# Kernel tuning notes

Hardware: AMD Instinct MI355X
Metric: run time of the kernel (lower is better)

Reference implementation:

```python
import jax, jax.numpy as jnp
import numpy as np
from jax.scipy.special import logsumexp

EPS = 0.1
MAX_ITER = 10
THRESH = 0.1


def setup_inputs() -> dict:
    key = jax.random.key(0)
    k1, k2 = jax.random.split(key)
    N, P, D = 16, 1024, 64
    y = jax.random.normal(k1, (N, P, D), dtype=jnp.float32)
    x = jax.random.normal(k2, (N, P, D), dtype=jnp.float32)
    return {"y": y, "x": x}


def reference(y, x):
    # Cost matrix |x_i - y_j|^2 summed over feature dim: (N, P1, P2)
    C = jnp.sum(jnp.abs(x[:, :, None, :] - y[:, None, :, :]) ** 2, axis=-1)
    N, P1, P2 = C.shape
    mu = jnp.full((N, P1), 1.0 / P1, dtype=C.dtype)
    nu = jnp.full((N, P2), 1.0 / P2, dtype=C.dtype)

    def M(u, v):
        # (-C + u_i + v_j) / eps
        return (-C + u[:, :, None] + v[:, None, :]) / EPS

    def body(carry, _):
        u, v, done = carry
        u_new = EPS * (jnp.log(mu + 1e-8) - logsumexp(M(u, v), axis=-1)) + u
        v_new = EPS * (jnp.log(nu + 1e-8) - logsumexp(M(u_new, v), axis=-2)) + v
        err = jnp.abs(u_new - u).sum(-1).mean()
        # emulate torch's early break: freeze updates once converged
        u2 = jnp.where(done, u, u_new)
        v2 = jnp.where(done, v, v_new)
        done2 = done | (err < THRESH)
        return (u2, v2, done2), None

    u0 = jnp.zeros_like(mu)
    v0 = jnp.zeros_like(nu)
    (u, v, _), _ = jax.lax.scan(body, (u0, v0, jnp.array(False)), None, length=MAX_ITER)
    pi = jnp.exp(M(u, v))  # transport plan (N, P1, P2)
    return pi
```

## Files before the change

### kernel.cpp

```cpp
#include <hip/hip_runtime.h>
#include <math.h>

#define NB 16
#define PP 1024
#define DD 64
#define MAX_ITER 10
#define RCH 16
#define NCH (PP / RCH)
#define NBLK (NB * NCH)
#define CH (NB * PP)

constexpr float EPSV    = 0.1f;
constexpr float SCALE_G = 20.0f;
constexpr float LOG2E   = 1.44269504088896340736f;
constexpr float LOG_MU  = -6.93146156597137f;
constexpr float THRESHV = 0.1f;

typedef short bf16x8 __attribute__((ext_vector_type(8)));
typedef float f32x16 __attribute__((ext_vector_type(16)));

__device__ __forceinline__ unsigned short f2bf(float f) {
  unsigned int u = __float_as_uint(f);
  return (unsigned short)((u + 0x7FFFu + ((u >> 16) & 1u)) >> 16);
}
__device__ __forceinline__ float bf2f(unsigned short h) {
  return __uint_as_float(((unsigned int)h) << 16);
}

__device__ __forceinline__ const bf16x8* frag(const unsigned short* pk, int g, int q, int l) {
  return (const bf16x8*)(pk + (((size_t)g * 4 + q) * 64 + l) * 8);
}

__global__ __launch_bounds__(256) void prep_kernel(
    const float* __restrict__ x, const float* __restrict__ y,
    unsigned short* __restrict__ xhp, unsigned short* __restrict__ xlp,
    unsigned short* __restrict__ yhp, unsigned short* __restrict__ ylp,
    float* __restrict__ nxs, float* __restrict__ nys)
{
  const int sel = blockIdx.x >> 9;
  const int row = (blockIdx.x & 511) * 32 + (threadIdx.x >> 3);
  const int q   = threadIdx.x & 7;

  const float* src = sel ? y : x;
  unsigned short* H = sel ? yhp : xhp;
  unsigned short* L = sel ? ylp : xlp;
  float* N          = sel ? nys : nxs;

  const float* p = src + (size_t)row * DD + q * 8;
  float4 v0 = *(const float4*)(p);
  float4 v1 = *(const float4*)(p + 4);

  float f[8] = {v0.x, v0.y, v0.z, v0.w, v1.x, v1.y, v1.z, v1.w};
  float nrm = 0.f;
  unsigned short hb[8], lb[8];
  #pragma unroll
  for (int k = 0; k < 8; ++k) {
    nrm = fmaf(f[k], f[k], nrm);
    unsigned short h = f2bf(f[k]);
    float res = f[k] - bf2f(h);
    hb[k] = h; lb[k] = f2bf(res);
  }
  nrm += __shfl_xor(nrm, 1);
  nrm += __shfl_xor(nrm, 2);
  nrm += __shfl_xor(nrm, 4);
  if (q == 0) N[row] = 10.0f * nrm;

  uint4 ho, lo;
  ho.x = hb[0] | ((unsigned)hb[1] << 16); ho.y = hb[2] | ((unsigned)hb[3] << 16);
  ho.z = hb[4] | ((unsigned)hb[5] << 16); ho.w = hb[6] | ((unsigned)hb[7] << 16);
  lo.x = lb[0] | ((unsigned)lb[1] << 16); lo.y = lb[2] | ((unsigned)lb[3] << 16);
  lo.z = lb[4] | ((unsigned)lb[5] << 16); lo.w = lb[6] | ((unsigned)lb[7] << 16);

  const int grp  = row >> 5;
  const int lane = (row & 31) + 32 * (q & 1);
  const size_t dst = (((size_t)grp * 4 + (q >> 1)) * 64 + lane) * 8;
  *(uint4*)(H + dst) = ho;
  *(uint4*)(L + dst) = lo;
}

__global__ __launch_bounds__(256) void compute_c_mfma(
    const unsigned short* __restrict__ xhp, const unsigned short* __restrict__ xlp,
    const float* __restrict__ nxs,
    const unsigned short* __restrict__ yhp, const unsigned short* __restrict__ ylp,
    const float* __restrict__ nys,
    float* __restrict__ Cs)
{
  const int n   = blockIdx.x & 15;
  const int ib  = (blockIdx.x >> 4) & 15;
  const int jb  = blockIdx.x >> 8;
  const int tid = threadIdx.x;
  const int l   = tid & 63;
  const int w   = tid >> 6;
  const int ih  = w & 1, jh = w >> 1;

  __shared__ float nxv[64];
  if (tid < 64) nxv[tid] = nxs[n * PP + ib * 64 + tid];
  __syncthreads();

  const int jg  = n * PP + jb * 64 + 32 * jh + (l & 31);
  const float nyv = nys[jg];

  const int gX = n * 32 + ib * 2 + ih;
  const int gY = n * 32 + jb * 2 + jh;

  f32x16 acc;
  #pragma unroll
  for (int z = 0; z < 16; ++z) acc[z] = 0.f;
  #pragma unroll
  for (int q = 0; q < 4; ++q) {
    bf16x8 Xh = *frag(xhp, gX, q, l);
    bf16x8 Xl = *frag(xlp, gX, q, l);
    bf16x8 Yh = *frag(yhp, gY, q, l);
    bf16x8 Yl = *frag(ylp, gY, q, l);
    acc = __builtin_amdgcn_mfma_f32_32x32x16_bf16(Xh, Yh, acc, 0, 0, 0);
    acc = __builtin_amdgcn_mfma_f32_32x32x16_bf16(Xh, Yl, acc, 0, 0, 0);
    acc = __builtin_amdgcn_mfma_f32_32x32x16_bf16(Xl, Yh, acc, 0, 0, 0);
  }

  const int irb  = 32 * ih + 4 * (l >> 5);
  const int jcol = jb * 64 + 32 * jh + (l & 31);
  #pragma unroll
  for (int r = 0; r < 16; ++r) {
    const int irel = irb + (r & 3) + 8 * (r >> 2);
    const size_t off = ((size_t)(n * PP + ib * 64 + irel)) * PP + jcol;
    Cs[off] = nxv[irel] + nyv - SCALE_G * acc[r];
  }
}

__global__ __launch_bounds__(256, 4) void iter_fused(
    const float* __restrict__ Cs, float* __restrict__ aG, const float* __restrict__ bG,
    float* __restrict__ pm, float* __restrict__ ps, float* __restrict__ errBlk,
    const int* __restrict__ doneFlags, int it)
{
  if (it > 0 && doneFlags[it - 1]) return;

  const int n   = blockIdx.x & 15;
  const int rc  = blockIdx.x >> 4;
  const int tid = threadIdx.x;
  const int l   = tid & 63;
  const int wv  = tid >> 6;

  __shared__ float bb[PP];
  __shared__ float aArr[RCH];
  __shared__ float dsum[RCH];

  if (it == 0) {
    *(float4*)&bb[tid * 4] = make_float4(0.f, 0.f, 0.f, 0.f);
  } else {
    *(float4*)&bb[tid * 4] = *(const float4*)(bG + n * PP + tid * 4);
  }
  __syncthreads();

  const int rbase = rc * RCH + 4 * wv;
  const float* cbase = Cs + ((size_t)(n * PP + rbase)) * PP;

  float4 bbv[4];
  #pragma unroll
  for (int s = 0; s < 4; ++s) bbv[s] = *(const float4*)&bb[s * 256 + l * 4];

  float4 tv[16];
  #pragma unroll
  for (int t = 0; t < 16; ++t) {
    const int r = t >> 2, s = t & 3;
    float4 c4 = *(const float4*)(cbase + (size_t)r * PP + s * 256 + l * 4);
    tv[t] = make_float4(bbv[s].x - c4.x, bbv[s].y - c4.y,
                        bbv[s].z - c4.z, bbv[s].w - c4.w);
  }

  float m0 = -INFINITY, m1 = -INFINITY, m2 = -INFINITY, m3 = -INFINITY;
  #pragma unroll
  for (int s = 0; s < 4; ++s) {
    m0 = fmaxf(m0, fmaxf(fmaxf(tv[s].x, tv[s].y), fmaxf(tv[s].z, tv[s].w)));
    m1 = fmaxf(m1, fmaxf(fmaxf(tv[4+s].x, tv[4+s].y), fmaxf(tv[4+s].z, tv[4+s].w)));
    m2 = fmaxf(m2, fmaxf(fmaxf(tv[8+s].x, tv[8+s].y), fmaxf(tv[8+s].z, tv[8+s].w)));
    m3 = fmaxf(m3, fmaxf(fmaxf(tv[12+s].x, tv[12+s].y), fmaxf(tv[12+s].z, tv[12+s].w)));
  }
  #pragma unroll
  for (int mask = 32; mask; mask >>= 1) {
    m0 = fmaxf(m0, __shfl_xor(m0, mask));
    m1 = fmaxf(m1, __shfl_xor(m1, mask));
    m2 = fmaxf(m2, __shfl_xor(m2, mask));
    m3 = fmaxf(m3, __shfl_xor(m3, mask));
  }

  float s0 = 0.f, s1 = 0.f, s2 = 0.f, s3 = 0.f;
  #pragma unroll
  for (int s = 0; s < 4; ++s) {
    s0 += exp2f((tv[s].x - m0) * LOG2E) + exp2f((tv[s].y - m0) * LOG2E)
        + exp2f((tv[s].z - m0) * LOG2E) + exp2f((tv[s].w - m0) * LOG2E);
    s1 += exp2f((tv[4+s].x - m1) * LOG2E) + exp2f((tv[4+s].y - m1) * LOG2E)
        + exp2f((tv[4+s].z - m1) * LOG2E) + exp2f((tv[4+s].w - m1) * LOG2E);
    s2 += exp2f((tv[8+s].x - m2) * LOG2E) + exp2f((tv[8+s].y - m2) * LOG2E)
        + exp2f((tv[8+s].z - m2) * LOG2E) + exp2f((tv[8+s].w - m2) * LOG2E);
    s3 += exp2f((tv[12+s].x - m3) * LOG2E) + exp2f((tv[12+s].y - m3) * LOG2E)
        + exp2f((tv[12+s].z - m3) * LOG2E) + exp2f((tv[12+s].w - m3) * LOG2E);
  }
  #pragma unroll
  for (int mask = 32; mask; mask >>= 1) {
    s0 += __shfl_xor(s0, mask);
    s1 += __shfl_xor(s1, mask);
    s2 += __shfl_xor(s2, mask);
    s3 += __shfl_xor(s3, mask);
  }

  if (l == 0) {
    float mg[4] = {m0, m1, m2, m3};
    float sg[4] = {s0, s1, s2, s3};
    #pragma unroll
    for (int g = 0; g < 4; ++g) {
      const int row = n * PP + rbase + g;
      float aOld = (it == 0) ? 0.f : aG[row];
      float an = LOG_MU - (mg[g] + logf(sg[g]));
      aG[row] = an;
      aArr[4 * wv + g] = an;
      dsum[4 * wv + g] = fabsf(an - aOld);
    }
  }
  __syncthreads();
  if (tid == 0) {
    float e = 0.f;
    #pragma unroll
    for (int r = 0; r < RCH; ++r) e += dsum[r];
    errBlk[blockIdx.x] = e;
  }

  const int c0 = tid * 4;
  const float* cb = Cs + ((size_t)(n * PP + rc * RCH)) * PP + c0;

  float cm0 = -INFINITY, cm1 = -INFINITY, cm2 = -INFINITY, cm3 = -INFINITY;
  #pragma unroll
  for (int r = 0; r < RCH; ++r) {
    float ar = aArr[r];
    float4 c4 = *(const float4*)(cb + (size_t)r * PP);
    cm0 = fmaxf(cm0, ar - c4.x);
    cm1 = fmaxf(cm1, ar - c4.y);
    cm2 = fmaxf(cm2, ar - c4.z);
    cm3 = fmaxf(cm3, ar - c4.w);
  }
  float cs0 = 0.f, cs1 = 0.f, cs2 = 0.f, cs3 = 0.f;
  #pragma unroll
  for (int r = 0; r < RCH; ++r) {
    float ar = aArr[r];
    float4 c4 = *(const float4*)(cb + (size_t)r * PP);
    cs0 += exp2f((ar - c4.x - cm0) * LOG2E);
    cs1 += exp2f((ar - c4.y - cm1) * LOG2E);
    cs2 += exp2f((ar - c4.z - cm2) * LOG2E);
    cs3 += exp2f((ar - c4.w - cm3) * LOG2E);
  }
  size_t off = ((size_t)(n * NCH + rc)) * PP + c0;
  *(float4*)(pm + off) = make_float4(cm0, cm1, cm2, cm3);
  *(float4*)(ps + off) = make_float4(cs0, cs1, cs2, cs3);
}

__global__ __launch_bounds__(256) void v_combine(
    const float* __restrict__ pm, const float* __restrict__ ps,
    float* __restrict__ bG, const float* __restrict__ errBlk,
    int* __restrict__ doneFlags, int it)
{
  if (it > 0 && doneFlags[it - 1]) {
    if (blockIdx.x == 0 && threadIdx.x == 0) doneFlags[it] = 1;
    return;
  }
  const int col = blockIdx.x * 256 + threadIdx.x;
  const int n = col >> 10, j = col & (PP - 1);
  const float* pmn = pm + (size_t)n * NCH * PP + j;
  const float* psn = ps + (size_t)n * NCH * PP + j;

  float m = -INFINITY, s = 0.f;
  #pragma unroll 8
  for (int c = 0; c < NCH; ++c) {
    float mc = pmn[(size_t)c * PP];
    float sc = psn[(size_t)c * PP];
    float mn = fmaxf(m, mc);
    s = fmaf(s, exp2f((m - mn) * LOG2E), sc * exp2f((mc - mn) * LOG2E));
    m = mn;
  }
  bG[col] = LOG_MU - (m + logf(s));

  if (blockIdx.x == 0) {
    __shared__ float red[4];
    float loc = 0.f;
    for (int t = threadIdx.x; t < NBLK; t += 256) loc += errBlk[t];
    #pragma unroll
    for (int off = 32; off > 0; off >>= 1) loc += __shfl_xor(loc, off);
    if ((threadIdx.x & 63) == 0) red[threadIdx.x >> 6] = loc;
    __syncthreads();
    if (threadIdx.x == 0) {
      float tot = red[0] + red[1] + red[2] + red[3];
      float err = tot * (EPSV / (float)NB);
      doneFlags[it] = (err < THRESHV) ? 1 : 0;
    }
  }
}

__global__ __launch_bounds__(256) void pi_mfma(
    const unsigned short* __restrict__ xhp, const unsigned short* __restrict__ xlp,
    const unsigned short* __restrict__ yhp, const unsigned short* __restrict__ ylp,
    const float* __restrict__ aG, const float* __restrict__ bG,
    const float* __restrict__ nxs, const float* __restrict__ nys,
    float* __restrict__ pi)
{
  const int n   = blockIdx.x & 15;
  const int ib  = (blockIdx.x >> 4) & 15;
  const int jb  = blockIdx.x >> 8;
  const int tid = threadIdx.x;
  const int l   = tid & 63;
  const int w   = tid >> 6;
  const int ih  = w & 1, jh = w >> 1;

  __shared__ float atv[64];
  if (tid < 64) {
    int gi = n * PP + ib * 64 + tid;
    atv[tid] = aG[gi] - nxs[gi];
  }
  __syncthreads();

  const int jg  = n * PP + jb * 64 + 32 * jh + (l & 31);
  const float btv = bG[jg] - nys[jg];

  const int gX = n * 32 + ib * 2 + ih;
  const int gY = n * 32 + jb * 2 + jh;

  f32x16 acc;
  #pragma unroll
  for (int z = 0; z < 16; ++z) acc[z] = 0.f;
  #pragma unroll
  for (int q = 0; q < 4; ++q) {
    bf16x8 Xh = *frag(xhp, gX, q, l);
    bf16x8 Xl = *frag(xlp, gX, q, l);
    bf16x8 Yh = *frag(yhp, gY, q, l);
    bf16x8 Yl = *frag(ylp, gY, q, l);
    acc = __builtin_amdgcn_mfma_f32_32x32x16_bf16(Xh, Yh, acc, 0, 0, 0);
    acc = __builtin_amdgcn_mfma_f32_32x32x16_bf16(Xh, Yl, acc, 0, 0, 0);
    acc = __builtin_amdgcn_mfma_f32_32x32x16_bf16(Xl, Yh, acc, 0, 0, 0);
  }

  const int irb  = 32 * ih + 4 * (l >> 5);
  const int jcol = jb * 64 + 32 * jh + (l & 31);
  #pragma unroll
  for (int r = 0; r < 16; ++r) {
    const int irel = irb + (r & 3) + 8 * (r >> 2);
    const size_t off = ((size_t)(n * PP + ib * 64 + irel)) * PP + jcol;
    pi[off] = exp2f((atv[irel] + btv + SCALE_G * acc[r]) * LOG2E);
  }
}

extern "C" void kernel_launch(void* const* d_in, const int* in_sizes, int n_in,
                              void* d_out, int out_size, void* d_ws, size_t ws_size,
                              hipStream_t stream)
{
  const float* y = (const float*)d_in[0];
  const float* x = (const float*)d_in[1];

  float* Cs = (float*)d_out;

  const size_t NE = (size_t)NB * PP * DD;
  unsigned short* xhp = (unsigned short*)d_ws;
  unsigned short* xlp = xhp + NE;
  unsigned short* yhp = xlp + NE;
  unsigned short* ylp = yhp + NE;
  float* pm = (float*)d_ws;
  float* ps = pm + (size_t)NB * NCH * PP;

  float* tail   = (float*)((char*)d_ws + 4 * NE * sizeof(unsigned short));
  float* nxs    = tail;
  float* nys    = nxs + CH;
  float* aG     = nys + CH;
  float* bG     = aG + CH;
  float* errBlk = bG + CH;
  int*   doneFl = (int*)(errBlk + NBLK);

  prep_kernel<<<1024, 256, 0, stream>>>(x, y, xhp, xlp, yhp, ylp, nxs, nys);
  compute_c_mfma<<<4096, 256, 0, stream>>>(xhp, xlp, nxs, yhp, ylp, nys, Cs);
  for (int it = 0; it < MAX_ITER; ++it) {
    iter_fused<<<NBLK, 256, 0, stream>>>(Cs, aG, bG, pm, ps, errBlk, doneFl, it);
    v_combine<<<NB * PP / 256, 256, 0, stream>>>(pm, ps, bG, errBlk, doneFl, it);
  }
  prep_kernel<<<1024, 256, 0, stream>>>(x, y, xhp, xlp, yhp, ylp, nxs, nys);
  pi_mfma<<<4096, 256, 0, stream>>>(xhp, xlp, yhp, ylp, aG, bG, nxs, nys, Cs);
}
```

Measured before the change: 365.7 us.

## Reuse register-held cost rows for column logsumexp partials via LDS reduction

```diff
diff --git a/kernel.cpp b/kernel.cpp
--- a/kernel.cpp
+++ b/kernel.cpp
@@ -141,6 +141,8 @@
   const int wv  = tid >> 6;
 
   __shared__ float bb[PP];
+  __shared__ float pmL[4][PP];
+  __shared__ float psL[4][PP];
   __shared__ float aArr[RCH];
   __shared__ float dsum[RCH];
 
@@ -224,32 +226,67 @@
     errBlk[blockIdx.x] = e;
   }
 
-  const int c0 = tid * 4;
-  const float* cb = Cs + ((size_t)(n * PP + rc * RCH)) * PP + c0;
-
-  float cm0 = -INFINITY, cm1 = -INFINITY, cm2 = -INFINITY, cm3 = -INFINITY;
-  #pragma unroll
-  for (int r = 0; r < RCH; ++r) {
-    float ar = aArr[r];
-    float4 c4 = *(const float4*)(cb + (size_t)r * PP);
-    cm0 = fmaxf(cm0, ar - c4.x);
-    cm1 = fmaxf(cm1, ar - c4.y);
-    cm2 = fmaxf(cm2, ar - c4.z);
-    cm3 = fmaxf(cm3, ar - c4.w);
-  }
-  float cs0 = 0.f, cs1 = 0.f, cs2 = 0.f, cs3 = 0.f;
-  #pragma unroll
-  for (int r = 0; r < RCH; ++r) {
-    float ar = aArr[r];
-    float4 c4 = *(const float4*)(cb + (size_t)r * PP);
-    cs0 += exp2f((ar - c4.x - cm0) * LOG2E);
-    cs1 += exp2f((ar - c4.y - cm1) * LOG2E);
-    cs2 += exp2f((ar - c4.z - cm2) * LOG2E);
-    cs3 += exp2f((ar - c4.w - cm3) * LOG2E);
-  }
-  size_t off = ((size_t)(n * NCH + rc)) * PP + c0;
-  *(float4*)(pm + off) = make_float4(cm0, cm1, cm2, cm3);
-  *(float4*)(ps + off) = make_float4(cs0, cs1, cs2, cs3);
+  float a4[4];
+  #pragma unroll
+  for (int g = 0; g < 4; ++g) a4[g] = aArr[4 * wv + g];
+
+  #pragma unroll
+  for (int s = 0; s < 4; ++s) {
+    float4 q0 = tv[s], q1 = tv[4 + s], q2 = tv[8 + s], q3 = tv[12 + s];
+    float4 b4 = bbv[s];
+    float4 c0 = make_float4(a4[0] - b4.x + q0.x, a4[0] - b4.y + q0.y,
+                            a4[0] - b4.z + q0.z, a4[0] - b4.w + q0.w);
+    float4 c1 = make_float4(a4[1] - b4.x + q1.x, a4[1] - b4.y + q1.y,
+                            a4[1] - b4.z + q1.z, a4[1] - b4.w + q1.w);
+    float4 c2 = make_float4(a4[2] - b4.x + q2.x, a4[2] - b4.y + q2.y,
+                            a4[2] - b4.z + q2.z, a4[2] - b4.w + q2.w);
+    float4 c3 = make_float4(a4[3] - b4.x + q3.x, a4[3] - b4.y + q3.y,
+                            a4[3] - b4.z + q3.z, a4[3] - b4.w + q3.w);
+    float4 mm = make_float4(fmaxf(fmaxf(c0.x, c1.x), fmaxf(c2.x, c3.x)),
+                            fmaxf(fmaxf(c0.y, c1.y), fmaxf(c2.y, c3.y)),
+                            fmaxf(fmaxf(c0.z, c1.z), fmaxf(c2.z, c3.z)),
+                            fmaxf(fmaxf(c0.w, c1.w), fmaxf(c2.w, c3.w)));
+    float4 ss;
+    ss.x = exp2f((c0.x - mm.x) * LOG2E) + exp2f((c1.x - mm.x) * LOG2E)
+         + exp2f((c2.x - mm.x) * LOG2E) + exp2f((c3.x - mm.x) * LOG2E);
+    ss.y = exp2f((c0.y - mm.y) * LOG2E) + exp2f((c1.y - mm.y) * LOG2E)
+         + exp2f((c2.y - mm.y) * LOG2E) + exp2f((c3.y - mm.y) * LOG2E);
+    ss.z = exp2f((c0.z - mm.z) * LOG2E) + exp2f((c1.z - mm.z) * LOG2E)
+         + exp2f((c2.z - mm.z) * LOG2E) + exp2f((c3.z - mm.z) * LOG2E);
+    ss.w = exp2f((c0.w - mm.w) * LOG2E) + exp2f((c1.w - mm.w) * LOG2E)
+         + exp2f((c2.w - mm.w) * LOG2E) + exp2f((c3.w - mm.w) * LOG2E);
+    *(float4*)&pmL[wv][s * 256 + l * 4] = mm;
+    *(float4*)&psL[wv][s * 256 + l * 4] = ss;
+  }
+  __syncthreads();
+
+  {
+    const int c0i = tid * 4;
+    float4 M0 = *(const float4*)&pmL[0][c0i];
+    float4 M1 = *(const float4*)&pmL[1][c0i];
+    float4 M2 = *(const float4*)&pmL[2][c0i];
+    float4 M3 = *(const float4*)&pmL[3][c0i];
+    float4 S0 = *(const float4*)&psL[0][c0i];
+    float4 S1 = *(const float4*)&psL[1][c0i];
+    float4 S2 = *(const float4*)&psL[2][c0i];
+    float4 S3 = *(const float4*)&psL[3][c0i];
+    float4 MM, SS;
+    MM.x = fmaxf(fmaxf(M0.x, M1.x), fmaxf(M2.x, M3.x));
+    MM.y = fmaxf(fmaxf(M0.y, M1.y), fmaxf(M2.y, M3.y));
+    MM.z = fmaxf(fmaxf(M0.z, M1.z), fmaxf(M2.z, M3.z));
+    MM.w = fmaxf(fmaxf(M0.w, M1.w), fmaxf(M2.w, M3.w));
+    SS.x = S0.x * exp2f((M0.x - MM.x) * LOG2E) + S1.x * exp2f((M1.x - MM.x) * LOG2E)
+         + S2.x * exp2f((M2.x - MM.x) * LOG2E) + S3.x * exp2f((M3.x - MM.x) * LOG2E);
+    SS.y = S0.y * exp2f((M0.y - MM.y) * LOG2E) + S1.y * exp2f((M1.y - MM.y) * LOG2E)
+         + S2.y * exp2f((M2.y - MM.y) * LOG2E) + S3.y * exp2f((M3.y - MM.y) * LOG2E);
+    SS.z = S0.z * exp2f((M0.z - MM.z) * LOG2E) + S1.z * exp2f((M1.z - MM.z) * LOG2E)
+         + S2.z * exp2f((M2.z - MM.z) * LOG2E) + S3.z * exp2f((M3.z - MM.z) * LOG2E);
+    SS.w = S0.w * exp2f((M0.w - MM.w) * LOG2E) + S1.w * exp2f((M1.w - MM.w) * LOG2E)
+         + S2.w * exp2f((M2.w - MM.w) * LOG2E) + S3.w * exp2f((M3.w - MM.w) * LOG2E);
+    size_t off = ((size_t)(n * NCH + rc)) * PP + c0i;
+    *(float4*)(pm + off) = MM;
+    *(float4*)(ps + off) = SS;
+  }
 }
 
 __global__ __launch_bounds__(256) void v_combine(
```

New measurement: 366.4 us. Within noise of the previous version (+0.2%).

## Compute column logsumexp partials from registers, avoiding a second cost-matrix read

Applied to the files above, without the earlier changes.

```diff
diff --git a/kernel.cpp b/kernel.cpp
--- a/kernel.cpp
+++ b/kernel.cpp
@@ -5,9 +5,9 @@
 #define PP 1024
 #define DD 64
 #define MAX_ITER 10
-#define RCH 16
-#define NCH (PP / RCH)
-#define NBLK (NB * NCH)
+#define RB 64
+#define NCHK (PP / RB)
+#define NBLK2 (NB * NCHK)
 #define CH (NB * PP)
 
 constexpr float EPSV    = 0.1f;
@@ -127,7 +127,7 @@
   }
 }
 
-__global__ __launch_bounds__(256, 4) void iter_fused(
+__global__ __launch_bounds__(512, 4) void iter_fused(
     const float* __restrict__ Cs, float* __restrict__ aG, const float* __restrict__ bG,
     float* __restrict__ pm, float* __restrict__ ps, float* __restrict__ errBlk,
     const int* __restrict__ doneFlags, int it)
@@ -141,115 +141,150 @@
   const int wv  = tid >> 6;
 
   __shared__ float bb[PP];
-  __shared__ float aArr[RCH];
-  __shared__ float dsum[RCH];
-
-  if (it == 0) {
-    *(float4*)&bb[tid * 4] = make_float4(0.f, 0.f, 0.f, 0.f);
-  } else {
-    *(float4*)&bb[tid * 4] = *(const float4*)(bG + n * PP + tid * 4);
+  __shared__ float pmL[8][PP + 8];
+  __shared__ float psL[8][PP + 8];
+  __shared__ float aArr[RB];
+  __shared__ float dsum[RB];
+
+  if (tid < 256) {
+    if (it == 0) {
+      *(float4*)&bb[tid * 4] = make_float4(0.f, 0.f, 0.f, 0.f);
+    } else {
+      *(float4*)&bb[tid * 4] = *(const float4*)(bG + n * PP + tid * 4);
+    }
   }
   __syncthreads();
 
-  const int rbase = rc * RCH + 4 * wv;
+  const int rbase = rc * RB + 8 * wv;
   const float* cbase = Cs + ((size_t)(n * PP + rbase)) * PP;
 
   float4 bbv[4];
   #pragma unroll
   for (int s = 0; s < 4; ++s) bbv[s] = *(const float4*)&bb[s * 256 + l * 4];
 
-  float4 tv[16];
-  #pragma unroll
-  for (int t = 0; t < 16; ++t) {
-    const int r = t >> 2, s = t & 3;
-    float4 c4 = *(const float4*)(cbase + (size_t)r * PP + s * 256 + l * 4);
-    tv[t] = make_float4(bbv[s].x - c4.x, bbv[s].y - c4.y,
-                        bbv[s].z - c4.z, bbv[s].w - c4.w);
-  }
-
-  float m0 = -INFINITY, m1 = -INFINITY, m2 = -INFINITY, m3 = -INFINITY;
+  float cm[16], cs[16];
+  #pragma unroll
+  for (int t = 0; t < 16; ++t) { cm[t] = -INFINITY; cs[t] = 0.f; }
+
+  #pragma unroll
+  for (int g = 0; g < 2; ++g) {
+    float4 tv[16];
+    #pragma unroll
+    for (int t = 0; t < 16; ++t) {
+      const int r = t >> 2, s = t & 3;
+      float4 c4 = *(const float4*)(cbase + (size_t)(4 * g + r) * PP + s * 256 + l * 4);
+      tv[t] = make_float4(bbv[s].x - c4.x, bbv[s].y - c4.y,
+                          bbv[s].z - c4.z, bbv[s].w - c4.w);
+    }
+
+    float m0 = -INFINITY, m1 = -INFINITY, m2 = -INFINITY, m3 = -INFINITY;
+    #pragma unroll
+    for (int s = 0; s < 4; ++s) {
+      m0 = fmaxf(m0, fmaxf(fmaxf(tv[s].x, tv[s].y), fmaxf(tv[s].z, tv[s].w)));
+      m1 = fmaxf(m1, fmaxf(fmaxf(tv[4+s].x, tv[4+s].y), fmaxf(tv[4+s].z, tv[4+s].w)));
+      m2 = fmaxf(m2, fmaxf(fmaxf(tv[8+s].x, tv[8+s].y), fmaxf(tv[8+s].z, tv[8+s].w)));
+      m3 = fmaxf(m3, fmaxf(fmaxf(tv[12+s].x, tv[12+s].y), fmaxf(tv[12+s].z, tv[12+s].w)));
+    }
+    #pragma unroll
+    for (int mask = 32; mask; mask >>= 1) {
+      m0 = fmaxf(m0, __shfl_xor(m0, mask));
+      m1 = fmaxf(m1, __shfl_xor(m1, mask));
+      m2 = fmaxf(m2, __shfl_xor(m2, mask));
+      m3 = fmaxf(m3, __shfl_xor(m3, mask));
+    }
+    float s0 = 0.f, s1 = 0.f, s2 = 0.f, s3 = 0.f;
+    #pragma unroll
+    for (int s = 0; s < 4; ++s) {
+      s0 += exp2f((tv[s].x - m0) * LOG2E) + exp2f((tv[s].y - m0) * LOG2E)
+          + exp2f((tv[s].z - m0) * LOG2E) + exp2f((tv[s].w - m0) * LOG2E);
+      s1 += exp2f((tv[4+s].x - m1) * LOG2E) + exp2f((tv[4+s].y - m1) * LOG2E)
+          + exp2f((tv[4+s].z - m1) * LOG2E) + exp2f((tv[4+s].w - m1) * LOG2E);
+      s2 += exp2f((tv[8+s].x - m2) * LOG2E) + exp2f((tv[8+s].y - m2) * LOG2E)
+          + exp2f((tv[8+s].z - m2) * LOG2E) + exp2f((tv[8+s].w - m2) * LOG2E);
+      s3 += exp2f((tv[12+s].x - m3) * LOG2E) + exp2f((tv[12+s].y - m3) * LOG2E)
+          + exp2f((tv[12+s].z - m3) * LOG2E) + exp2f((tv[12+s].w - m3) * LOG2E);
+    }
+    #pragma unroll
+    for (int mask = 32; mask; mask >>= 1) {
+      s0 += __shfl_xor(s0, mask);
+      s1 += __shfl_xor(s1, mask);
+      s2 += __shfl_xor(s2, mask);
+      s3 += __shfl_xor(s3, mask);
+    }
+
+    float an[4];
+    an[0] = LOG_MU - (m0 + logf(s0));
+    an[1] = LOG_MU - (m1 + logf(s1));
+    an[2] = LOG_MU - (m2 + logf(s2));
+    an[3] = LOG_MU - (m3 + logf(s3));
+
+    if (l == 0) {
+      #pragma unroll
+      for (int r = 0; r < 4; ++r) {
+        const int lrow = 8 * wv + 4 * g + r;
+        const int grow = n * PP + rc * RB + lrow;
+        float aOld = (it == 0) ? 0.f : aG[grow];
+        aG[grow] = an[r];
+        aArr[lrow] = an[r];
+        dsum[lrow] = fabsf(an[r] - aOld);
+      }
+    }
+
+    #pragma unroll
+    for (int s = 0; s < 4; ++s) {
+      float4 q0 = tv[s], q1 = tv[4 + s], q2 = tv[8 + s], q3 = tv[12 + s];
+      float4 b4 = bbv[s];
+      float bc[4] = {b4.x, b4.y, b4.z, b4.w};
+      float t0[4] = {q0.x, q0.y, q0.z, q0.w};
+      float t1[4] = {q1.x, q1.y, q1.z, q1.w};
+      float t2[4] = {q2.x, q2.y, q2.z, q2.w};
+      float t3[4] = {q3.x, q3.y, q3.z, q3.w};
+      #pragma unroll
+      for (int k = 0; k < 4; ++k) {
+        float c0 = an[0] - bc[k] + t0[k];
+        float c1 = an[1] - bc[k] + t1[k];
+        float c2 = an[2] - bc[k] + t2[k];
+        float c3 = an[3] - bc[k] + t3[k];
+        float mn = fmaxf(fmaxf(c0, c1), fmaxf(c2, c3));
+        float sn = exp2f((c0 - mn) * LOG2E) + exp2f((c1 - mn) * LOG2E)
+                 + exp2f((c2 - mn) * LOG2E) + exp2f((c3 - mn) * LOG2E);
+        const int idx = s * 4 + k;
+        float M = fmaxf(cm[idx], mn);
+        cs[idx] = cs[idx] * exp2f((cm[idx] - M) * LOG2E) + sn * exp2f((mn - M) * LOG2E);
+        cm[idx] = M;
+      }
+    }
+  }
+
   #pragma unroll
   for (int s = 0; s < 4; ++s) {
-    m0 = fmaxf(m0, fmaxf(fmaxf(tv[s].x, tv[s].y), fmaxf(tv[s].z, tv[s].w)));
-    m1 = fmaxf(m1, fmaxf(fmaxf(tv[4+s].x, tv[4+s].y), fmaxf(tv[4+s].z, tv[4+s].w)));
-    m2 = fmaxf(m2, fmaxf(fmaxf(tv[8+s].x, tv[8+s].y), fmaxf(tv[8+s].z, tv[8+s].w)));
-    m3 = fmaxf(m3, fmaxf(fmaxf(tv[12+s].x, tv[12+s].y), fmaxf(tv[12+s].z, tv[12+s].w)));
-  }
-  #pragma unroll
-  for (int mask = 32; mask; mask >>= 1) {
-    m0 = fmaxf(m0, __shfl_xor(m0, mask));
-    m1 = fmaxf(m1, __shfl_xor(m1, mask));
-    m2 = fmaxf(m2, __shfl_xor(m2, mask));
-    m3 = fmaxf(m3, __shfl_xor(m3, mask));
-  }
-
-  float s0 = 0.f, s1 = 0.f, s2 = 0.f, s3 = 0.f;
-  #pragma unroll
-  for (int s = 0; s < 4; ++s) {
-    s0 += exp2f((tv[s].x - m0) * LOG2E) + exp2f((tv[s].y - m0) * LOG2E)
-        + exp2f((tv[s].z - m0) * LOG2E) + exp2f((tv[s].w - m0) * LOG2E);
-    s1 += exp2f((tv[4+s].x - m1) * LOG2E) + exp2f((tv[4+s].y - m1) * LOG2E)
-        + exp2f((tv[4+s].z - m1) * LOG2E) + exp2f((tv[4+s].w - m1) * LOG2E);
-    s2 += exp2f((tv[8+s].x - m2) * LOG2E) + exp2f((tv[8+s].y - m2) * LOG2E)
-        + exp2f((tv[8+s].z - m2) * LOG2E) + exp2f((tv[8+s].w - m2) * LOG2E);
-    s3 += exp2f((tv[12+s].x - m3) * LOG2E) + exp2f((tv[12+s].y - m3) * LOG2E)
-        + exp2f((tv[12+s].z - m3) * LOG2E) + exp2f((tv[12+s].w - m3) * LOG2E);
-  }
-  #pragma unroll
-  for (int mask = 32; mask; mask >>= 1) {
-    s0 += __shfl_xor(s0, mask);
-    s1 += __shfl_xor(s1, mask);
-    s2 += __shfl_xor(s2, mask);
-    s3 += __shfl_xor(s3, mask);
-  }
-
-  if (l == 0) {
-    float mg[4] = {m0, m1, m2, m3};
-    float sg[4] = {s0, s1, s2, s3};
-    #pragma unroll
-    for (int g = 0; g < 4; ++g) {
-      const int row = n * PP + rbase + g;
-      float aOld = (it == 0) ? 0.f : aG[row];
-      float an = LOG_MU - (mg[g] + logf(sg[g]));
-      aG[row] = an;
-      aArr[4 * wv + g] = an;
-      dsum[4 * wv + g] = fabsf(an - aOld);
-    }
+    *(float4*)&pmL[wv][s * 256 + l * 4] = make_float4(cm[s*4+0], cm[s*4+1], cm[s*4+2], cm[s*4+3]);
+    *(float4*)&psL[wv][s * 256 + l * 4] = make_float4(cs[s*4+0], cs[s*4+1], cs[s*4+2], cs[s*4+3]);
   }
   __syncthreads();
+
   if (tid == 0) {
     float e = 0.f;
     #pragma unroll
-    for (int r = 0; r < RCH; ++r) e += dsum[r];
+    for (int r = 0; r < RB; ++r) e += dsum[r];
     errBlk[blockIdx.x] = e;
   }
 
-  const int c0 = tid * 4;
-  const float* cb = Cs + ((size_t)(n * PP + rc * RCH)) * PP + c0;
-
-  float cm0 = -INFINITY, cm1 = -INFINITY, cm2 = -INFINITY, cm3 = -INFINITY;
-  #pragma unroll
-  for (int r = 0; r < RCH; ++r) {
-    float ar = aArr[r];
-    float4 c4 = *(const float4*)(cb + (size_t)r * PP);
-    cm0 = fmaxf(cm0, ar - c4.x);
-    cm1 = fmaxf(cm1, ar - c4.y);
-    cm2 = fmaxf(cm2, ar - c4.z);
-    cm3 = fmaxf(cm3, ar - c4.w);
-  }
-  float cs0 = 0.f, cs1 = 0.f, cs2 = 0.f, cs3 = 0.f;
-  #pragma unroll
-  for (int r = 0; r < RCH; ++r) {
-    float ar = aArr[r];
-    float4 c4 = *(const float4*)(cb + (size_t)r * PP);
-    cs0 += exp2f((ar - c4.x - cm0) * LOG2E);
-    cs1 += exp2f((ar - c4.y - cm1) * LOG2E);
-    cs2 += exp2f((ar - c4.z - cm2) * LOG2E);
-    cs3 += exp2f((ar - c4.w - cm3) * LOG2E);
-  }
-  size_t off = ((size_t)(n * NCH + rc)) * PP + c0;
-  *(float4*)(pm + off) = make_float4(cm0, cm1, cm2, cm3);
-  *(float4*)(ps + off) = make_float4(cs0, cs1, cs2, cs3);
+  {
+    #pragma unroll
+    for (int u = 0; u < 2; ++u) {
+      const int j = tid * 2 + u;
+      float M = pmL[0][j];
+      #pragma unroll
+      for (int w2 = 1; w2 < 8; ++w2) M = fmaxf(M, pmL[w2][j]);
+      float S = 0.f;
+      #pragma unroll
+      for (int w2 = 0; w2 < 8; ++w2) S += psL[w2][j] * exp2f((pmL[w2][j] - M) * LOG2E);
+      const size_t off = ((size_t)(n * NCHK + rc)) * PP + j;
+      pm[off] = M;
+      ps[off] = S;
+    }
+  }
 }
 
 __global__ __launch_bounds__(256) void v_combine(
@@ -263,12 +298,12 @@
   }
   const int col = blockIdx.x * 256 + threadIdx.x;
   const int n = col >> 10, j = col & (PP - 1);
-  const float* pmn = pm + (size_t)n * NCH * PP + j;
-  const float* psn = ps + (size_t)n * NCH * PP + j;
+  const float* pmn = pm + (size_t)n * NCHK * PP + j;
+  const float* psn = ps + (size_t)n * NCHK * PP + j;
 
   float m = -INFINITY, s = 0.f;
   #pragma unroll 8
-  for (int c = 0; c < NCH; ++c) {
+  for (int c = 0; c < NCHK; ++c) {
     float mc = pmn[(size_t)c * PP];
     float sc = psn[(size_t)c * PP];
     float mn = fmaxf(m, mc);
@@ -279,8 +314,7 @@
 
   if (blockIdx.x == 0) {
     __shared__ float red[4];
-    float loc = 0.f;
-    for (int t = threadIdx.x; t < NBLK; t += 256) loc += errBlk[t];
+    float loc = errBlk[threadIdx.x];
     #pragma unroll
     for (int off = 32; off > 0; off >>= 1) loc += __shfl_xor(loc, off);
     if ((threadIdx.x & 63) == 0) red[threadIdx.x >> 6] = loc;
@@ -360,7 +394,7 @@
   unsigned short* yhp = xlp + NE;
   unsigned short* ylp = yhp + NE;
   float* pm = (float*)d_ws;
-  float* ps = pm + (size_t)NB * NCH * PP;
+  float* ps = pm + (size_t)NB * NCHK * PP;
 
   float* tail   = (float*)((char*)d_ws + 4 * NE * sizeof(unsigned short));
   float* nxs    = tail;
@@ -368,12 +402,12 @@
   float* aG     = nys + CH;
   float* bG     = aG + CH;
   float* errBlk = bG + CH;
-  int*   doneFl = (int*)(errBlk + NBLK);
+  int*   doneFl = (int*)(errBlk + NBLK2);
 
   prep_kernel<<<1024, 256, 0, stream>>>(x, y, xhp, xlp, yhp, ylp, nxs, nys);
   compute_c_mfma<<<4096, 256, 0, stream>>>(xhp, xlp, nxs, yhp, ylp, nys, Cs);
   for (int it = 0; it < MAX_ITER; ++it) {
-    iter_fused<<<NBLK, 256, 0, stream>>>(Cs, aG, bG, pm, ps, errBlk, doneFl, it);
+    iter_fused<<<NBLK2, 512, 0, stream>>>(Cs, aG, bG, pm, ps, errBlk, doneFl, it);
     v_combine<<<NB * PP / 256, 256, 0, stream>>>(pm, ps, bG, errBlk, doneFl, it);
   }
   prep_kernel<<<1024, 256, 0, stream>>>(x, y, xhp, xlp, yhp, ylp, nxs, nys);
```

Result: slower. 484.3 us (+32.4%).
